# Optimization experiments

Hardware: AMD Instinct MI355X
Metric: run time of the kernel (lower is better)

Reference implementation:

```python
import jax, jax.numpy as jnp
import numpy as np

IN_SIZE = 4096
OUT_SIZE = 4096
BATCH = 256
NNZ = (IN_SIZE * OUT_SIZE) // 2


def setup_inputs() -> dict:
    key = jax.random.key(0)
    k_x, k_row, k_col, k_val = jax.random.split(key, 4)
    X = jax.random.normal(k_x, (BATCH, IN_SIZE), dtype=jnp.float32)
    rows = jax.random.randint(k_row, (NNZ,), 0, IN_SIZE, dtype=jnp.int64)
    cols = jax.random.randint(k_col, (NNZ,), 0, OUT_SIZE, dtype=jnp.int64)
    idx = jnp.stack([rows, cols], axis=1)  # [NNZ, 2] (input_idx, output_idx)
    lim = 1.0 / np.sqrt(IN_SIZE)
    val = jax.random.uniform(k_val, (NNZ,), dtype=jnp.float32, minval=-lim, maxval=lim)
    bias = jnp.zeros((OUT_SIZE,), dtype=jnp.float32)
    return {"X": X, "idx": idx, "val": val, "bias": bias}


def reference(X, idx, val, bias):
    # Scatter the COO sparse weight into a dense [IN, OUT] matrix.
    # .add accumulates duplicate indices, matching tf.SparseTensor matmul semantics.
    W = jnp.zeros((IN_SIZE, OUT_SIZE), dtype=val.dtype).at[idx[:, 0], idx[:, 1]].add(val)
    # Z = X @ W + b  (original: transpose(sparse_matmul(W^T, X^T)) + b)
    Z = jnp.dot(X, W) + bias
    return jax.nn.relu(Z)
```

## Files before the change

### kernel.cpp

```cpp
#include <hip/hip_runtime.h>
#include <hip/hip_bf16.h>

#define IN_SIZE 4096
#define OUT_SIZE 4096
#define BATCH 256
#define NNZ ((IN_SIZE * OUT_SIZE) / 2)

#define NB    512
#define BBIN  512
#define EPB   (NNZ / BBIN)
#define CHUNK 4096
#define NCH   (EPB / CHUNK)
#define REP    8
#define SUBCAP 3072
#define CAP    (REP * SUBCAP)
#define SPLITK 8

typedef float f32x4 __attribute__((ext_vector_type(4)));
typedef short s16x8 __attribute__((ext_vector_type(8)));

static const size_t OFF_XBF  = 0;
static const size_t OFF_WTBF = (size_t)2 << 20;
static const size_t OFF_PART = (size_t)34 << 20;
static const size_t OFF_BIN  = (size_t)66 << 20;
static const size_t OFF_CNT  = (size_t)114 << 20;
static const size_t WS_NEED  = OFF_CNT + (size_t)REP * NB * 4;

__device__ __forceinline__ short bfbits(float f) {
    __hip_bfloat16 h = __float2bfloat16(f);
    return __builtin_bit_cast(short, h);
}
__device__ __forceinline__ s16x8 pack8(f32x4 lo, f32x4 hi) {
    s16x8 r;
    r[0] = bfbits(lo[0]); r[1] = bfbits(lo[1]); r[2] = bfbits(lo[2]); r[3] = bfbits(lo[3]);
    r[4] = bfbits(hi[0]); r[5] = bfbits(hi[1]); r[6] = bfbits(hi[2]); r[7] = bfbits(hi[3]);
    return r;
}
__device__ __forceinline__ unsigned packel(int r, int c, float v) {
    return ((unsigned)(unsigned short)bfbits(v) << 15) |
           (unsigned)((c & 7) * IN_SIZE + r);
}
__device__ __forceinline__ float unpackv(unsigned p) {
    return __uint_as_float((p >> 15) << 16);
}

__device__ __forceinline__ void scan512(const unsigned* h, unsigned* out,
                                        unsigned* wsum, int t) {
    const int lane = t & 63, wid = t >> 6;
    const unsigned a0 = h[2 * t], a1 = h[2 * t + 1];
    const unsigned s = a0 + a1;
    unsigned inc = s;
#pragma unroll
    for (int d = 1; d < 64; d <<= 1) {
        const unsigned n = __shfl_up(inc, d);
        if (lane >= d) inc += n;
    }
    if (lane == 63) wsum[wid] = inc;
    __syncthreads();
    unsigned wpre = 0;
#pragma unroll
    for (int i = 0; i < 4; ++i)
        if (i < wid) wpre += wsum[i];
    const unsigned ex = wpre + inc - s;
    out[2 * t]     = ex;
    out[2 * t + 1] = ex + a0;
    __syncthreads();
}

__global__ __launch_bounds__(256) void k_xcvt(const float* __restrict__ X,
                                              s16x8* __restrict__ Xb) {
    const int i8 = blockIdx.x * 256 + threadIdx.x;
    const f32x4 lo = reinterpret_cast<const f32x4*>(X)[2 * i8];
    const f32x4 hi = reinterpret_cast<const f32x4*>(X)[2 * i8 + 1];
    Xb[i8] = pack8(lo, hi);
}

__global__ __launch_bounds__(256) void k_bin(const int4* __restrict__ idx4,
                                             const float2* __restrict__ val2,
                                             unsigned* __restrict__ cnt,
                                             unsigned* __restrict__ binned) {
    __shared__ unsigned hist[NB], start[NB], curb[NB], wsum[4];
    __shared__ uint2 st[CHUNK];
    const int t = threadIdx.x, blk = blockIdx.x;
    const int rep = blk & (REP - 1);

    for (int ch = 0; ch < NCH; ++ch) {
        hist[2 * t] = 0; hist[2 * t + 1] = 0;
        __syncthreads();
        const int pbase = (blk * EPB + ch * CHUNK) / 2;
        unsigned eb[16], er[16], epk[16];
#pragma unroll
        for (int j = 0; j < 8; ++j) {
            const int4 e   = idx4[pbase + t + 256 * j];
            const float2 v = val2[pbase + t + 256 * j];
            eb[2 * j]      = ((unsigned)e.y) >> 3;
            epk[2 * j]     = packel(e.x, e.y, v.x);
            er[2 * j]      = atomicAdd(&hist[eb[2 * j]], 1u);
            eb[2 * j + 1]  = ((unsigned)e.w) >> 3;
            epk[2 * j + 1] = packel(e.z, e.w, v.y);
            er[2 * j + 1]  = atomicAdd(&hist[eb[2 * j + 1]], 1u);
        }
        __syncthreads();
        scan512(hist, start, wsum, t);
        {
            const unsigned h0 = hist[2 * t], h1 = hist[2 * t + 1];
            const unsigned r0 = h0 ? atomicAdd(&cnt[rep * NB + 2 * t], h0) : 0u;
            const unsigned r1 = h1 ? atomicAdd(&cnt[rep * NB + 2 * t + 1], h1) : 0u;
            curb[2 * t]     = (unsigned)(2 * t) * CAP + rep * SUBCAP + r0;
            curb[2 * t + 1] = (unsigned)(2 * t + 1) * CAP + rep * SUBCAP + r1;
        }
        __syncthreads();
#pragma unroll
        for (int j = 0; j < 16; ++j) {
            const unsigned lp = start[eb[j]] + er[j];
            st[lp] = make_uint2(curb[eb[j]] + er[j], epk[j]);
        }
        __syncthreads();
#pragma unroll
        for (int j = 0; j < 16; ++j) {
            const uint2 s = st[t + 256 * j];
            binned[s.x] = s.y;
        }
        __syncthreads();
    }
}

__global__ __launch_bounds__(1024) void k_accum(const unsigned* __restrict__ binned,
                                                const unsigned* __restrict__ cnt,
                                                s16x8* __restrict__ Wtb8) {
    __shared__ float acc[8 * IN_SIZE];
    const int t = threadIdx.x, b = blockIdx.x;
    f32x4* a4 = reinterpret_cast<f32x4*>(acc);
#pragma unroll
    for (int j = 0; j < (8 * IN_SIZE / 4) / 1024; ++j)
        a4[t + 1024 * j] = (f32x4){0.f, 0.f, 0.f, 0.f};
    __syncthreads();
    const unsigned base = (unsigned)b * CAP;
#pragma unroll 1
    for (int r = 0; r < REP; ++r) {
        const unsigned n  = cnt[r * NB + b];
        const unsigned rb = base + r * SUBCAP;
        for (unsigned i = t; i < n; i += 1024) {
            const unsigned p = binned[rb + i];
            atomicAdd(&acc[p & 32767u], unpackv(p));
        }
    }
    __syncthreads();
    s16x8* dst = Wtb8 + (size_t)b * (8 * IN_SIZE / 8);
#pragma unroll
    for (int j = 0; j < (8 * IN_SIZE / 8) / 1024; ++j) {
        const int i8 = t + 1024 * j;
        dst[i8] = pack8(a4[2 * i8], a4[2 * i8 + 1]);
    }
}

__global__ __launch_bounds__(256) void k_gemm(const short* __restrict__ A,
                                              const short* __restrict__ B,
                                              float* __restrict__ part) {
    const int l = threadIdx.x & 63, w = threadIdx.x >> 6;
    const int bm = blockIdx.y * 128, bn = blockIdx.x * 32, kz = blockIdx.z;
    const int lr = l & 15, kg = (l >> 4) * 8;
    const int kb = kz * (IN_SIZE / SPLITK);

    const short* pA[2];
    const short* pB[2];
#pragma unroll
    for (int mi = 0; mi < 2; ++mi)
        pA[mi] = A + (size_t)(bm + w * 32 + mi * 16 + lr) * IN_SIZE + kb + kg;
#pragma unroll
    for (int ni = 0; ni < 2; ++ni)
        pB[ni] = B + (size_t)(bn + ni * 16 + lr) * IN_SIZE + kb + kg;

    f32x4 acc[2][2] = {};
    s16x8 a[2], b[2];
#pragma unroll
    for (int mi = 0; mi < 2; ++mi) { a[mi] = *reinterpret_cast<const s16x8*>(pA[mi]); pA[mi] += 32; }
#pragma unroll
    for (int ni = 0; ni < 2; ++ni) { b[ni] = *reinterpret_cast<const s16x8*>(pB[ni]); pB[ni] += 32; }

#pragma unroll 2
    for (int s = 0; s < (IN_SIZE / SPLITK) / 32 - 1; ++s) {
        s16x8 na[2], nb[2];
#pragma unroll
        for (int mi = 0; mi < 2; ++mi) { na[mi] = *reinterpret_cast<const s16x8*>(pA[mi]); pA[mi] += 32; }
#pragma unroll
        for (int ni = 0; ni < 2; ++ni) { nb[ni] = *reinterpret_cast<const s16x8*>(pB[ni]); pB[ni] += 32; }
#pragma unroll
        for (int mi = 0; mi < 2; ++mi)
#pragma unroll
            for (int ni = 0; ni < 2; ++ni)
                acc[mi][ni] = __builtin_amdgcn_mfma_f32_16x16x32_bf16(a[mi], b[ni], acc[mi][ni], 0, 0, 0);
#pragma unroll
        for (int mi = 0; mi < 2; ++mi) a[mi] = na[mi];
#pragma unroll
        for (int ni = 0; ni < 2; ++ni) b[ni] = nb[ni];
    }
#pragma unroll
    for (int mi = 0; mi < 2; ++mi)
#pragma unroll
        for (int ni = 0; ni < 2; ++ni)
            acc[mi][ni] = __builtin_amdgcn_mfma_f32_16x16x32_bf16(a[mi], b[ni], acc[mi][ni], 0, 0, 0);

    float* P = part + (size_t)kz * (BATCH * OUT_SIZE);
#pragma unroll
    for (int mi = 0; mi < 2; ++mi)
#pragma unroll
        for (int ni = 0; ni < 2; ++ni) {
            const int col = bn + ni * 16 + lr;
            const int r0 = bm + w * 32 + mi * 16 + ((l >> 4) << 2);
#pragma unroll
            for (int rr = 0; rr < 4; ++rr)
                P[(size_t)(r0 + rr) * OUT_SIZE + col] = acc[mi][ni][rr];
        }
}

__global__ __launch_bounds__(256) void k_reduce(const float* __restrict__ part,
                                                const float* __restrict__ bias,
                                                float* __restrict__ Z) {
    const int i4 = blockIdx.x * 256 + threadIdx.x;
    f32x4 s = reinterpret_cast<const f32x4*>(part)[i4];
#pragma unroll
    for (int r = 1; r < SPLITK; ++r) {
        const f32x4 p = reinterpret_cast<const f32x4*>(part + (size_t)r * BATCH * OUT_SIZE)[i4];
#pragma unroll
        for (int k = 0; k < 4; ++k) s[k] += p[k];
    }
    const f32x4 bv = reinterpret_cast<const f32x4*>(bias)[i4 & (OUT_SIZE / 4 - 1)];
    f32x4 o;
#pragma unroll
    for (int k = 0; k < 4; ++k) o[k] = fmaxf(s[k] + bv[k], 0.f);
    reinterpret_cast<f32x4*>(Z)[i4] = o;
}

#define SC_BLOCKS 1024
__global__ __launch_bounds__(256) void scatter_t(const int2* __restrict__ idx2,
                                                 const float* __restrict__ val,
                                                 float* __restrict__ Wt) {
    const int stride = SC_BLOCKS * 256;
    int i = blockIdx.x * 256 + threadIdx.x;
#pragma unroll 1
    for (int iter = 0; iter < NNZ / (4 * SC_BLOCKS * 256); ++iter) {
        const int2 e0 = idx2[i];
        const int2 e1 = idx2[i + stride];
        const int2 e2 = idx2[i + 2 * stride];
        const int2 e3 = idx2[i + 3 * stride];
        const float v0 = val[i], v1 = val[i + stride], v2 = val[i + 2 * stride], v3 = val[i + 3 * stride];
        atomicAdd(&Wt[e0.y * IN_SIZE + e0.x], v0);
        atomicAdd(&Wt[e1.y * IN_SIZE + e1.x], v1);
        atomicAdd(&Wt[e2.y * IN_SIZE + e2.x], v2);
        atomicAdd(&Wt[e3.y * IN_SIZE + e3.x], v3);
        i += 4 * stride;
    }
}

__global__ __launch_bounds__(256) void gemm_mfma(const float* __restrict__ X,
                                                 const float* __restrict__ Wt,
                                                 const float* __restrict__ bias,
                                                 float* __restrict__ Z) {
    const int l = threadIdx.x & 63, w = threadIdx.x >> 6;
    const int bm = blockIdx.y * 128, bn = blockIdx.x * 32;
    const int lr = l & 15, kg = (l >> 4) * 8;
    const float* pA[2];
    const float* pB[2];
#pragma unroll
    for (int mi = 0; mi < 2; ++mi) pA[mi] = X + (bm + w * 32 + mi * 16 + lr) * IN_SIZE + kg;
#pragma unroll
    for (int ni = 0; ni < 2; ++ni) pB[ni] = Wt + (bn + ni * 16 + lr) * IN_SIZE + kg;
    f32x4 acc[2][2] = {};
#pragma unroll 2
    for (int k0 = 0; k0 < IN_SIZE; k0 += 32) {
        s16x8 a[2], b[2];
#pragma unroll
        for (int mi = 0; mi < 2; ++mi) {
            const f32x4 lo = *reinterpret_cast<const f32x4*>(pA[mi]);
            const f32x4 hi = *reinterpret_cast<const f32x4*>(pA[mi] + 4);
            a[mi] = pack8(lo, hi); pA[mi] += 32;
        }
#pragma unroll
        for (int ni = 0; ni < 2; ++ni) {
            const f32x4 lo = *reinterpret_cast<const f32x4*>(pB[ni]);
            const f32x4 hi = *reinterpret_cast<const f32x4*>(pB[ni] + 4);
            b[ni] = pack8(lo, hi); pB[ni] += 32;
        }
#pragma unroll
        for (int mi = 0; mi < 2; ++mi)
#pragma unroll
            for (int ni = 0; ni < 2; ++ni)
                acc[mi][ni] = __builtin_amdgcn_mfma_f32_16x16x32_bf16(a[mi], b[ni], acc[mi][ni], 0, 0, 0);
    }
#pragma unroll
    for (int mi = 0; mi < 2; ++mi)
#pragma unroll
        for (int ni = 0; ni < 2; ++ni) {
            const int col = bn + ni * 16 + lr;
            const float bv = bias[col];
            const int r0 = bm + w * 32 + mi * 16 + ((l >> 4) << 2);
#pragma unroll
            for (int rr = 0; rr < 4; ++rr)
                Z[(r0 + rr) * OUT_SIZE + col] = fmaxf(acc[mi][ni][rr] + bv, 0.f);
        }
}

extern "C" void kernel_launch(void* const* d_in, const int* in_sizes, int n_in,
                              void* d_out, int out_size, void* d_ws, size_t ws_size,
                              hipStream_t stream) {
    const float* X    = (const float*)d_in[0];
    const int*   idx  = (const int*)d_in[1];
    const float* val  = (const float*)d_in[2];
    const float* bias = (const float*)d_in[3];
    float* Z = (float*)d_out;
    char*  ws = (char*)d_ws;

    if (ws_size >= WS_NEED) {
        s16x8*    Xb     = (s16x8*)(ws + OFF_XBF);
        short*    Wtb    = (short*)(ws + OFF_WTBF);
        float*    part   = (float*)(ws + OFF_PART);
        unsigned* binned = (unsigned*)(ws + OFF_BIN);
        unsigned* cnt    = (unsigned*)(ws + OFF_CNT);

        hipMemsetAsync(cnt, 0, (size_t)REP * NB * 4, stream);
        k_xcvt<<<(BATCH * IN_SIZE) / (256 * 8), 256, 0, stream>>>(X, Xb);
        k_bin<<<BBIN, 256, 0, stream>>>((const int4*)idx, (const float2*)val, cnt, binned);
        k_accum<<<NB, 1024, 0, stream>>>(binned, cnt, (s16x8*)Wtb);
        dim3 gg(OUT_SIZE / 32, BATCH / 128, SPLITK);
        k_gemm<<<gg, 256, 0, stream>>>((const short*)Xb, Wtb, part);
        k_reduce<<<(BATCH * OUT_SIZE) / (256 * 4), 256, 0, stream>>>(part, bias, Z);
    } else {
        float* Wt = (float*)d_ws;
        hipMemsetAsync(Wt, 0, (size_t)IN_SIZE * OUT_SIZE * sizeof(float), stream);
        scatter_t<<<SC_BLOCKS, 256, 0, stream>>>((const int2*)idx, val, Wt);
        dim3 grid(OUT_SIZE / 32, BATCH / 128);
        gemm_mfma<<<grid, 256, 0, stream>>>(X, Wt, bias, Z);
    }
}
```

Before: 273.4 us.

## Stage GEMM tiles through LDS with 64x64 blocks and halve split-K

The bf16 MFMA GEMM now loads 64x64x64 tiles of X and W^T into padded shared memory, with register prefetch of the next tile, and the four waves share them. Before, each wave streamed its fragments straight from global memory. Split-K drops from 8 to 4, which halves the fp32 partial buffer that is written and then re-read by the reduce kernel, and the workspace offsets are compacted to match. The binning kernel also launches twice as many blocks, each handling fewer elements. The trade-off is two barriers per k-step, a larger LDS footprint, and less parallelism in the GEMM grid.

```diff
diff --git a/kernel.cpp b/kernel.cpp
--- a/kernel.cpp
+++ b/kernel.cpp
@@ -7,14 +7,19 @@
 #define NNZ ((IN_SIZE * OUT_SIZE) / 2)
 
 #define NB    512
-#define BBIN  512
+#define BBIN  1024
 #define EPB   (NNZ / BBIN)
 #define CHUNK 4096
 #define NCH   (EPB / CHUNK)
 #define REP    8
 #define SUBCAP 3072
 #define CAP    (REP * SUBCAP)
-#define SPLITK 8
+#define SPLITK 4
+
+#define BM 64
+#define BN 64
+#define BK 64
+#define LDA 72
 
 typedef float f32x4 __attribute__((ext_vector_type(4)));
 typedef short s16x8 __attribute__((ext_vector_type(8)));
@@ -22,8 +27,8 @@
 static const size_t OFF_XBF  = 0;
 static const size_t OFF_WTBF = (size_t)2 << 20;
 static const size_t OFF_PART = (size_t)34 << 20;
-static const size_t OFF_BIN  = (size_t)66 << 20;
-static const size_t OFF_CNT  = (size_t)114 << 20;
+static const size_t OFF_BIN  = (size_t)50 << 20;
+static const size_t OFF_CNT  = (size_t)98 << 20;
 static const size_t WS_NEED  = OFF_CNT + (size_t)REP * NB * 4;
 
 __device__ __forceinline__ short bfbits(float f) {
@@ -157,57 +162,75 @@
 __global__ __launch_bounds__(256) void k_gemm(const short* __restrict__ A,
                                               const short* __restrict__ B,
                                               float* __restrict__ part) {
-    const int l = threadIdx.x & 63, w = threadIdx.x >> 6;
-    const int bm = blockIdx.y * 128, bn = blockIdx.x * 32, kz = blockIdx.z;
+    __shared__ short As[BM * LDA];
+    __shared__ short Bs[BN * LDA];
+    const int t  = threadIdx.x;
+    const int l  = t & 63;
+    const int w  = t >> 6;
+    const int wm = (w >> 1) * 32, wn = (w & 1) * 32;
     const int lr = l & 15, kg = (l >> 4) * 8;
-    const int kb = kz * (IN_SIZE / SPLITK);
-
-    const short* pA[2];
-    const short* pB[2];
+    const int bn = blockIdx.x * BN, bm = blockIdx.y * BM;
+    const size_t kb = (size_t)blockIdx.z * (IN_SIZE / SPLITK);
+
+    const int r0s = t >> 3;
+    const int r1s = r0s + 32;
+    const int c0  = (t & 7) * 8;
+    const short* gA0 = A + (size_t)(bm + r0s) * IN_SIZE + kb + c0;
+    const short* gA1 = A + (size_t)(bm + r1s) * IN_SIZE + kb + c0;
+    const short* gB0 = B + (size_t)(bn + r0s) * IN_SIZE + kb + c0;
+    const short* gB1 = B + (size_t)(bn + r1s) * IN_SIZE + kb + c0;
+
+    f32x4 acc[2][2] = {};
+    s16x8 ra0 = *reinterpret_cast<const s16x8*>(gA0);
+    s16x8 ra1 = *reinterpret_cast<const s16x8*>(gA1);
+    s16x8 rb0 = *reinterpret_cast<const s16x8*>(gB0);
+    s16x8 rb1 = *reinterpret_cast<const s16x8*>(gB1);
+
+    const int NIT = (IN_SIZE / SPLITK) / BK;
+#pragma unroll 1
+    for (int it = 0; it < NIT; ++it) {
+        __syncthreads();
+        *reinterpret_cast<s16x8*>(&As[r0s * LDA + c0]) = ra0;
+        *reinterpret_cast<s16x8*>(&As[r1s * LDA + c0]) = ra1;
+        *reinterpret_cast<s16x8*>(&Bs[r0s * LDA + c0]) = rb0;
+        *reinterpret_cast<s16x8*>(&Bs[r1s * LDA + c0]) = rb1;
+        __syncthreads();
+        if (it + 1 < NIT) {
+            const int o = (it + 1) * BK;
+            ra0 = *reinterpret_cast<const s16x8*>(gA0 + o);
+            ra1 = *reinterpret_cast<const s16x8*>(gA1 + o);
+            rb0 = *reinterpret_cast<const s16x8*>(gB0 + o);
+            rb1 = *reinterpret_cast<const s16x8*>(gB1 + o);
+        }
+        s16x8 af[2][2], bf[2][2];
+#pragma unroll
+        for (int kk = 0; kk < 2; ++kk) {
+#pragma unroll
+            for (int mi = 0; mi < 2; ++mi)
+                af[kk][mi] = *reinterpret_cast<const s16x8*>(
+                    &As[(wm + mi * 16 + lr) * LDA + kk * 32 + kg]);
+#pragma unroll
+            for (int ni = 0; ni < 2; ++ni)
+                bf[kk][ni] = *reinterpret_cast<const s16x8*>(
+                    &Bs[(wn + ni * 16 + lr) * LDA + kk * 32 + kg]);
+        }
+#pragma unroll
+        for (int kk = 0; kk < 2; ++kk)
+#pragma unroll
+            for (int mi = 0; mi < 2; ++mi)
+#pragma unroll
+                for (int ni = 0; ni < 2; ++ni)
+                    acc[mi][ni] = __builtin_amdgcn_mfma_f32_16x16x32_bf16(
+                        af[kk][mi], bf[kk][ni], acc[mi][ni], 0, 0, 0);
+    }
+
+    float* P = part + (size_t)blockIdx.z * (BATCH * OUT_SIZE);
 #pragma unroll
     for (int mi = 0; mi < 2; ++mi)
-        pA[mi] = A + (size_t)(bm + w * 32 + mi * 16 + lr) * IN_SIZE + kb + kg;
-#pragma unroll
-    for (int ni = 0; ni < 2; ++ni)
-        pB[ni] = B + (size_t)(bn + ni * 16 + lr) * IN_SIZE + kb + kg;
-
-    f32x4 acc[2][2] = {};
-    s16x8 a[2], b[2];
-#pragma unroll
-    for (int mi = 0; mi < 2; ++mi) { a[mi] = *reinterpret_cast<const s16x8*>(pA[mi]); pA[mi] += 32; }
-#pragma unroll
-    for (int ni = 0; ni < 2; ++ni) { b[ni] = *reinterpret_cast<const s16x8*>(pB[ni]); pB[ni] += 32; }
-
-#pragma unroll 2
-    for (int s = 0; s < (IN_SIZE / SPLITK) / 32 - 1; ++s) {
-        s16x8 na[2], nb[2];
-#pragma unroll
-        for (int mi = 0; mi < 2; ++mi) { na[mi] = *reinterpret_cast<const s16x8*>(pA[mi]); pA[mi] += 32; }
-#pragma unroll
-        for (int ni = 0; ni < 2; ++ni) { nb[ni] = *reinterpret_cast<const s16x8*>(pB[ni]); pB[ni] += 32; }
-#pragma unroll
-        for (int mi = 0; mi < 2; ++mi)
-#pragma unroll
-            for (int ni = 0; ni < 2; ++ni)
-                acc[mi][ni] = __builtin_amdgcn_mfma_f32_16x16x32_bf16(a[mi], b[ni], acc[mi][ni], 0, 0, 0);
-#pragma unroll
-        for (int mi = 0; mi < 2; ++mi) a[mi] = na[mi];
-#pragma unroll
-        for (int ni = 0; ni < 2; ++ni) b[ni] = nb[ni];
-    }
-#pragma unroll
-    for (int mi = 0; mi < 2; ++mi)
-#pragma unroll
-        for (int ni = 0; ni < 2; ++ni)
-            acc[mi][ni] = __builtin_amdgcn_mfma_f32_16x16x32_bf16(a[mi], b[ni], acc[mi][ni], 0, 0, 0);
-
-    float* P = part + (size_t)kz * (BATCH * OUT_SIZE);
-#pragma unroll
-    for (int mi = 0; mi < 2; ++mi)
 #pragma unroll
         for (int ni = 0; ni < 2; ++ni) {
-            const int col = bn + ni * 16 + lr;
-            const int r0 = bm + w * 32 + mi * 16 + ((l >> 4) << 2);
+            const int col = bn + wn + ni * 16 + lr;
+            const int r0 = bm + wm + mi * 16 + ((l >> 4) << 2);
 #pragma unroll
             for (int rr = 0; rr < 4; ++rr)
                 P[(size_t)(r0 + rr) * OUT_SIZE + col] = acc[mi][ni][rr];
@@ -322,7 +345,7 @@
         k_xcvt<<<(BATCH * IN_SIZE) / (256 * 8), 256, 0, stream>>>(X, Xb);
         k_bin<<<BBIN, 256, 0, stream>>>((const int4*)idx, (const float2*)val, cnt, binned);
         k_accum<<<NB, 1024, 0, stream>>>(binned, cnt, (s16x8*)Wtb);
-        dim3 gg(OUT_SIZE / 32, BATCH / 128, SPLITK);
+        dim3 gg(OUT_SIZE / BN, BATCH / BM, SPLITK);
         k_gemm<<<gg, 256, 0, stream>>>((const short*)Xb, Wtb, part);
         k_reduce<<<(BATCH * OUT_SIZE) / (256 * 4), 256, 0, stream>>>(part, bias, Z);
     } else {
```

New measurement: 227.3 us. -16.8%, faster.
